# Optimization experiments

Hardware: AMD Instinct MI355X
Metric: run time of the kernel (lower is better)

Reference implementation:

```python
import jax, jax.numpy as jnp
import numpy as np

H = 768       # hidden_dim
NH = 12       # num_heads
HD = H // NH  # head_dim = 64


def setup_inputs() -> dict:
    key = jax.random.key(0)
    ks = jax.random.split(key, 5)
    scale = 1.0 / np.sqrt(H)
    x = jax.random.normal(ks[0], (16, 1024, H), dtype=jnp.float32)
    W_qkv = jax.random.normal(ks[1], (H, 3 * H), dtype=jnp.float32) * scale
    b_qkv = jnp.zeros((3 * H,), dtype=jnp.float32)
    W_proj = jax.random.normal(ks[2], (H, H), dtype=jnp.float32) * scale
    b_proj = jnp.zeros((H,), dtype=jnp.float32)
    return {"x": x, "W_qkv": W_qkv, "b_qkv": b_qkv, "W_proj": W_proj, "b_proj": b_proj}


def reference(x, W_qkv, b_qkv, W_proj, b_proj):
    bsz, seq_len, hidden = x.shape
    qkv = x @ W_qkv + b_qkv                              # [B,S,3H]
    q, k, v = jnp.split(qkv, 3, axis=-1)
    def heads(t):
        return t.reshape(bsz, seq_len, NH, HD).transpose(0, 2, 1, 3)  # [B,NH,S,HD]
    q, k, v = heads(q), heads(k), heads(v)
    scores = jnp.einsum('bhqd,bhkd->bhqk', q, k) / jnp.sqrt(jnp.float32(HD))
    causal = jnp.tril(jnp.ones((seq_len, seq_len), dtype=bool))
    scores = jnp.where(causal, scores, jnp.finfo(scores.dtype).min)
    attn = jax.nn.softmax(scores, axis=-1)
    out = jnp.einsum('bhqk,bhkd->bhqd', attn, v)         # [B,NH,S,HD]
    out = out.transpose(0, 2, 1, 3).reshape(bsz, seq_len, hidden)
    return out @ W_proj + b_proj
```

## Files before the change

### kernel.cpp

```cpp
#include <hip/hip_runtime.h>

#define H 768
#define NH 12
#define HD 64
#define BSZ 16
#define SEQ 1024
#define MTOK (BSZ * SEQ)
#define N3H (3 * H)

typedef __attribute__((ext_vector_type(8))) short bf16x8;
typedef __attribute__((ext_vector_type(4))) float f32x4;
typedef __attribute__((ext_vector_type(16))) float f32x16;
typedef __attribute__((ext_vector_type(8))) unsigned short us8;
typedef __attribute__((ext_vector_type(4))) unsigned short us4;

__device__ __forceinline__ unsigned short f2bf(float f) {
    union { float f; unsigned u; } v; v.f = f;
    unsigned r = v.u + 0x7fffu + ((v.u >> 16) & 1u);
    return (unsigned short)(r >> 16);
}

typedef __attribute__((address_space(1))) const unsigned int gu32_t;
typedef __attribute__((address_space(3))) unsigned int lu32_t;
__device__ __forceinline__ void glds16(const void* g, void* l) {
    __builtin_amdgcn_global_load_lds((gu32_t*)g, (lu32_t*)l, 16, 0, 0);
}

__global__ __launch_bounds__(256) void cvt_bf16(
    const float* __restrict__ in, unsigned short* __restrict__ out, int n)
{
    int i = (blockIdx.x * 256 + threadIdx.x) * 8;
    if (i >= n) return;
    float4 a = *(const float4*)(in + i);
    float4 b = *(const float4*)(in + i + 4);
    us8 o;
    o[0]=f2bf(a.x); o[1]=f2bf(a.y); o[2]=f2bf(a.z); o[3]=f2bf(a.w);
    o[4]=f2bf(b.x); o[5]=f2bf(b.y); o[6]=f2bf(b.z); o[7]=f2bf(b.w);
    *(us8*)(out + i) = o;
}

__global__ __launch_bounds__(256) void tconv_bf16(
    const float* __restrict__ in, unsigned short* __restrict__ out, int Kd, int Nd)
{
    __shared__ float tile[64][65];
    int t = threadIdx.x;
    int n0 = blockIdx.x * 64, k0 = blockIdx.y * 64;
    #pragma unroll
    for (int r = 0; r < 4; ++r) {
        int kl = r * 16 + (t >> 4);
        float4 v = *(const float4*)(&in[(size_t)(k0 + kl) * Nd + n0 + (t & 15) * 4]);
        tile[kl][(t & 15) * 4 + 0] = v.x; tile[kl][(t & 15) * 4 + 1] = v.y;
        tile[kl][(t & 15) * 4 + 2] = v.z; tile[kl][(t & 15) * 4 + 3] = v.w;
    }
    __syncthreads();
    int nl = t >> 2, kc = (t & 3) * 16;
    us8 o0, o1;
    #pragma unroll
    for (int kk = 0; kk < 8; ++kk) o0[kk] = f2bf(tile[kc + kk][nl]);
    #pragma unroll
    for (int kk = 0; kk < 8; ++kk) o1[kk] = f2bf(tile[kc + 8 + kk][nl]);
    size_t ob = (size_t)(n0 + nl) * Kd + k0 + kc;
    *(us8*)(&out[ob]) = o0;
    *(us8*)(&out[ob + 8]) = o1;
}

__global__ __launch_bounds__(256) void gemm_bf16(
    const unsigned short* __restrict__ A, const unsigned short* __restrict__ BT,
    const float* __restrict__ bias, void* __restrict__ Cout,
    int M, int N, int K, int write_f32)
{
    __shared__ char lds[32768];
    char* As = lds;
    char* Bs = lds + 16384;
    const char* Ac = (const char*)A;
    const char* Bc = (const char*)BT;
    int t = threadIdx.x;
    int l = t & 63, w = t >> 6;
    int l16 = l & 15, l4 = l >> 4;
    int wm = w >> 1, wn = w & 1;

    int chunk = (int)gridDim.x >> 3;
    int lin = (blockIdx.x & 7) * chunk + (blockIdx.x >> 3);
    int nbx = N >> 7;
    int bx = lin % nbx, by = lin / nbx;
    int rowBase = by * 128, colBase = bx * 128;

    f32x4 acc[4][4];
    #pragma unroll
    for (int i = 0; i < 4; ++i)
        #pragma unroll
        for (int j = 0; j < 4; ++j) acc[i][j] = (f32x4){0, 0, 0, 0};

    for (int k0 = 0; k0 < K; k0 += 64) {
        #pragma unroll
        for (int i = 0; i < 4; ++i) {
            int c = t + i * 256;
            int row = c >> 3;
            int src = ((c & 7) * 16) ^ ((row & 7) << 4);
            glds16(Ac + ((size_t)(rowBase + row) * K + k0) * 2 + src, As + c * 16);
            glds16(Bc + ((size_t)(colBase + row) * K + k0) * 2 + src, Bs + c * 16);
        }
        asm volatile("s_waitcnt vmcnt(0)" ::: "memory");
        __builtin_amdgcn_s_barrier();

        #pragma unroll
        for (int kh = 0; kh < 2; ++kh) {
            bf16x8 af[4], bfr[4];
            #pragma unroll
            for (int mi = 0; mi < 4; ++mi) {
                int row = wm * 64 + mi * 16 + l16;
                af[mi] = *(const bf16x8*)(As + row * 128 + ((l4 * 16 + kh * 64) ^ ((row & 7) << 4)));
            }
            #pragma unroll
            for (int ni = 0; ni < 4; ++ni) {
                int row = wn * 64 + ni * 16 + l16;
                bfr[ni] = *(const bf16x8*)(Bs + row * 128 + ((l4 * 16 + kh * 64) ^ ((row & 7) << 4)));
            }
            #pragma unroll
            for (int mi = 0; mi < 4; ++mi)
                #pragma unroll
                for (int ni = 0; ni < 4; ++ni)
                    acc[mi][ni] = __builtin_amdgcn_mfma_f32_16x16x32_bf16(
                        af[mi], bfr[ni], acc[mi][ni], 0, 0, 0);
        }
        __builtin_amdgcn_s_barrier();
    }

    #pragma unroll
    for (int ni = 0; ni < 4; ++ni) {
        int col = colBase + wn * 64 + ni * 16 + l16;
        float bb = bias ? bias[col] : 0.f;
        #pragma unroll
        for (int mi = 0; mi < 4; ++mi) {
            #pragma unroll
            for (int j = 0; j < 4; ++j) {
                int row = rowBase + wm * 64 + mi * 16 + l4 * 4 + j;
                float v = acc[mi][ni][j] + bb;
                if (write_f32) ((float*)Cout)[(size_t)row * N + col] = v;
                else ((unsigned short*)Cout)[(size_t)row * N + col] = f2bf(v);
            }
        }
    }
}

__global__ __launch_bounds__(256) void vtrans(
    const unsigned short* __restrict__ qkvb, unsigned short* __restrict__ vt)
{
    __shared__ char tile[64 * 128];
    int t = threadIdx.x;
    int st = blockIdx.x, h = blockIdx.y, b = blockIdx.z;
    int s0 = st * 64;
    {
        int s = t >> 2, dc = (t & 3) * 16;
        size_t g = (size_t)(b * SEQ + s0 + s) * N3H + 2 * H + h * HD + dc;
        us8 v0 = *(const us8*)(&qkvb[g]);
        us8 v1 = *(const us8*)(&qkvb[g + 8]);
        *(us8*)(tile + s * 128 + ((dc * 2) ^ ((s & 7) << 4))) = v0;
        *(us8*)(tile + s * 128 + ((dc * 2 + 16) ^ ((s & 7) << 4))) = v1;
    }
    __syncthreads();
    int d = t >> 2, sc = (t & 3) * 16;
    us8 o0, o1;
    #pragma unroll
    for (int kk = 0; kk < 8; ++kk) {
        int s = sc + kk;
        o0[kk] = *(const unsigned short*)(tile + s * 128 + ((d * 2) ^ ((s & 7) << 4)));
    }
    #pragma unroll
    for (int kk = 0; kk < 8; ++kk) {
        int s = sc + 8 + kk;
        o1[kk] = *(const unsigned short*)(tile + s * 128 + ((d * 2) ^ ((s & 7) << 4)));
    }
    size_t ob = ((size_t)((b * NH + h) * 64 + d)) * SEQ + s0 + sc;
    *(us8*)(&vt[ob]) = o0;
    *(us8*)(&vt[ob + 8]) = o1;
}

__global__ __launch_bounds__(256, 4) void attn_mfma(
    const unsigned short* __restrict__ qkvb,
    const unsigned short* __restrict__ vt,
    unsigned short* __restrict__ aout)
{
    __shared__ char lds[32768];
    char* Kbuf = lds;
    char* Vbuf = lds + 16384;
    int t = threadIdx.x;
    int l = t & 63, w = t >> 6;
    int l31 = l & 31, b5 = l >> 5;

    int lin = ((blockIdx.x & 7) * 192) + (blockIdx.x >> 3);
    int qb = 7 - (lin & 7);
    int bh = lin >> 3;
    int h = bh % NH, b = bh / NH;

    int wq = qb * 128 + w * 32;
    int sw31 = (l31 & 7) << 4;
    int nt = 2 * qb + 2;
    int bhh = b * NH + h;
    const char* qkvc = (const char*)qkvb;
    const char* vtc  = (const char*)vt;

    bf16x8 qB[4];
    {
        const unsigned short* qrow =
            qkvb + (size_t)(b * SEQ + wq + l31) * N3H + h * HD + b5 * 8;
        #pragma unroll
        for (int m = 0; m < 4; ++m) qB[m] = *(const bf16x8*)(qrow + m * 16);
    }

    auto STAGE = [&](int kt, int bi) {
        #pragma unroll
        for (int i = 0; i < 2; ++i) {
            int c = t + i * 256;
            int row = c >> 3;
            int src = ((c & 7) * 16) ^ ((row & 7) << 4);
            glds16(qkvc + ((size_t)(b * SEQ + kt * 64 + row) * N3H + H + h * HD) * 2 + src,
                   Kbuf + bi * 8192 + c * 16);
        }
        #pragma unroll
        for (int i = 0; i < 2; ++i) {
            int c = t + i * 256;
            int row = c >> 3;
            int src = ((c & 7) * 16) ^ ((row & 7) << 4);
            glds16(vtc + (((size_t)(bhh * 64 + row)) * SEQ + kt * 64) * 2 + src,
                   Vbuf + bi * 8192 + c * 16);
        }
    };

    STAGE(0, 0);
    __syncthreads();

    f32x16 o0, o1;
    #pragma unroll
    for (int r = 0; r < 16; ++r) { o0[r] = 0.f; o1[r] = 0.f; }
    float mrun = -1e30f, lrun = 0.f;

    for (int kt = 0; kt < nt; ++kt) {
        int bi = kt & 1;
        if (kt + 1 < nt) {
            STAGE(kt + 1, bi ^ 1);
            asm volatile("s_waitcnt vmcnt(4)" ::: "memory");
        } else {
            asm volatile("s_waitcnt vmcnt(0)" ::: "memory");
        }
        __builtin_amdgcn_s_barrier();

        int ktbase = kt * 64;
        if (ktbase <= wq + 31) {
            const char* Kb = Kbuf + bi * 8192;
            const char* Vb = Vbuf + bi * 8192;

            f32x16 s[2];
            __builtin_amdgcn_s_setprio(1);
            #pragma unroll
            for (int st2 = 0; st2 < 2; ++st2) {
                f32x16 acc;
                #pragma unroll
                for (int r = 0; r < 16; ++r) acc[r] = 0.f;
                #pragma unroll
                for (int m = 0; m < 4; ++m) {
                    int row = st2 * 32 + l31;
                    bf16x8 kf = *(const bf16x8*)(Kb + row * 128 + ((m * 32 + b5 * 16) ^ sw31));
                    acc = __builtin_amdgcn_mfma_f32_32x32x16_bf16(kf, qB[m], acc, 0, 0, 0);
                }
                s[st2] = acc;
            }
            __builtin_amdgcn_s_setprio(0);

            if (ktbase + 63 > wq) {
                int q = wq + l31;
                #pragma unroll
                for (int st2 = 0; st2 < 2; ++st2)
                    #pragma unroll
                    for (int r = 0; r < 16; ++r) {
                        int key = ktbase + st2 * 32 + (r & 3) + 8 * (r >> 2) + 4 * b5;
                        if (key > q) s[st2][r] = -3e38f;
                    }
            }

            float mx = s[0][0];
            #pragma unroll
            for (int r = 1; r < 16; ++r) mx = fmaxf(mx, s[0][r]);
            #pragma unroll
            for (int r = 0; r < 16; ++r) mx = fmaxf(mx, s[1][r]);
            mx = fmaxf(mx, __shfl_xor(mx, 32, 64));
            float mnew = fmaxf(mrun, mx * 0.125f);
            float sc = __expf(mrun - mnew);
            mrun = mnew;
            float rs = 0.f;
            #pragma unroll
            for (int st2 = 0; st2 < 2; ++st2)
                #pragma unroll
                for (int r = 0; r < 16; ++r) {
                    float p = __expf(fmaf(s[st2][r], 0.125f, -mnew));
                    s[st2][r] = p;
                    rs += p;
                }
            rs += __shfl_xor(rs, 32, 64);
            lrun = lrun * sc + rs;
            #pragma unroll
            for (int r = 0; r < 16; ++r) { o0[r] *= sc; o1[r] *= sc; }

            bf16x8 pB[4];
            #pragma unroll
            for (int wd = 0; wd < 4; ++wd) {
                int st2 = wd >> 1, hf = (wd & 1) * 8;
                unsigned pk0 = (unsigned)f2bf(s[st2][hf + 0]) | ((unsigned)f2bf(s[st2][hf + 1]) << 16);
                unsigned pk1 = (unsigned)f2bf(s[st2][hf + 2]) | ((unsigned)f2bf(s[st2][hf + 3]) << 16);
                unsigned pk2 = (unsigned)f2bf(s[st2][hf + 4]) | ((unsigned)f2bf(s[st2][hf + 5]) << 16);
                unsigned pk3 = (unsigned)f2bf(s[st2][hf + 6]) | ((unsigned)f2bf(s[st2][hf + 7]) << 16);
                unsigned snd0 = b5 ? pk0 : pk2;
                unsigned snd1 = b5 ? pk1 : pk3;
                unsigned r0 = (unsigned)__shfl_xor((int)snd0, 32, 64);
                unsigned r1 = (unsigned)__shfl_xor((int)snd1, 32, 64);
                union { unsigned u[4]; bf16x8 v; } cvt;
                cvt.u[0] = b5 ? r0 : pk0;
                cvt.u[1] = b5 ? r1 : pk1;
                cvt.u[2] = b5 ? pk2 : r0;
                cvt.u[3] = b5 ? pk3 : r1;
                pB[wd] = cvt.v;
            }

            __builtin_amdgcn_s_setprio(1);
            #pragma unroll
            for (int wd = 0; wd < 4; ++wd) {
                bf16x8 v0 = *(const bf16x8*)(Vb + l31 * 128 + ((wd * 32 + b5 * 16) ^ sw31));
                o0 = __builtin_amdgcn_mfma_f32_32x32x16_bf16(v0, pB[wd], o0, 0, 0, 0);
                bf16x8 v1 = *(const bf16x8*)(Vb + (32 + l31) * 128 + ((wd * 32 + b5 * 16) ^ sw31));
                o1 = __builtin_amdgcn_mfma_f32_32x32x16_bf16(v1, pB[wd], o1, 0, 0, 0);
            }
            __builtin_amdgcn_s_setprio(0);
        }
        __builtin_amdgcn_s_barrier();
    }

    float inv = 1.f / lrun;
    size_t tok = (size_t)(b * SEQ + wq + l31);
    #pragma unroll
    for (int g = 0; g < 4; ++g) {
        us4 w0, w1;
        #pragma unroll
        for (int j = 0; j < 4; ++j) {
            w0[j] = f2bf(o0[g * 4 + j] * inv);
            w1[j] = f2bf(o1[g * 4 + j] * inv);
        }
        int d0 = g * 8 + b5 * 4;
        *(us4*)(&aout[tok * H + h * HD + d0]) = w0;
        *(us4*)(&aout[tok * H + h * HD + 32 + d0]) = w1;
    }
}

extern "C" void kernel_launch(void* const* d_in, const int* in_sizes, int n_in,
                              void* d_out, int out_size, void* d_ws, size_t ws_size,
                              hipStream_t stream) {
    const float* x      = (const float*)d_in[0];
    const float* W_qkv  = (const float*)d_in[1];
    const float* b_qkv  = (const float*)d_in[2];
    const float* W_proj = (const float*)d_in[3];
    const float* b_proj = (const float*)d_in[4];
    float* outp = (float*)d_out;

    char* ws = (char*)d_ws;
    unsigned short* xbf    = (unsigned short*)ws;  ws += (size_t)MTOK * H * 2;
    unsigned short* wqkvT  = (unsigned short*)ws;  ws += (size_t)N3H * H * 2;
    unsigned short* wprojT = (unsigned short*)ws;  ws += (size_t)H * H * 2;
    unsigned short* qkvb   = (unsigned short*)ws;  ws += (size_t)MTOK * N3H * 2;
    unsigned short* vtb    = (unsigned short*)ws;  ws += (size_t)BSZ * NH * 64 * SEQ * 2;
    unsigned short* aob    = (unsigned short*)ws;

    cvt_bf16<<<(MTOK * H) / (256 * 8), 256, 0, stream>>>(x, xbf, MTOK * H);
    tconv_bf16<<<dim3(N3H / 64, H / 64), 256, 0, stream>>>(W_qkv, wqkvT, H, N3H);
    tconv_bf16<<<dim3(H / 64, H / 64), 256, 0, stream>>>(W_proj, wprojT, H, H);

    gemm_bf16<<<(N3H / 128) * (MTOK / 128), 256, 0, stream>>>(
        xbf, wqkvT, b_qkv, qkvb, MTOK, N3H, H, 0);

    vtrans<<<dim3(SEQ / 64, NH, BSZ), 256, 0, stream>>>(qkvb, vtb);

    attn_mfma<<<(SEQ / 128) * NH * BSZ, 256, 0, stream>>>(qkvb, vtb, aob);

    gemm_bf16<<<(H / 128) * (MTOK / 128), 256, 0, stream>>>(
        aob, wprojT, b_proj, (void*)outp, MTOK, H, H, 1);
}
```

Measured before the change: 317.8 us.

## Double-buffer GEMM LDS loads, fold Q scaling into GEMM, lazy softmax rescale

The GEMM now double-buffers its LDS tiles, so the next K-tile's global-to-LDS loads are issued before the MFMAs on the current tile, and it waits only on the older loads. The QKV GEMM epilogue multiplies Q columns by 1/sqrt(HD), which removes the per-score scaling in attention. The attention softmax skips the running-max rescale of the output and row sum unless some lane's max grew by more than a threshold, trading bounded exp growth for fewer multiplies. LDS per GEMM block doubles to 64KB, which may reduce occupancy.

```diff
diff --git a/kernel.cpp b/kernel.cpp
--- a/kernel.cpp
+++ b/kernel.cpp
@@ -67,11 +67,9 @@
 __global__ __launch_bounds__(256) void gemm_bf16(
     const unsigned short* __restrict__ A, const unsigned short* __restrict__ BT,
     const float* __restrict__ bias, void* __restrict__ Cout,
-    int M, int N, int K, int write_f32)
+    int M, int N, int K, int write_f32, int qscale_end)
 {
-    __shared__ char lds[32768];
-    char* As = lds;
-    char* Bs = lds + 16384;
+    __shared__ char lds[65536];
     const char* Ac = (const char*)A;
     const char* Bc = (const char*)BT;
     int t = threadIdx.x;
@@ -91,7 +89,9 @@
         #pragma unroll
         for (int j = 0; j < 4; ++j) acc[i][j] = (f32x4){0, 0, 0, 0};
 
-    for (int k0 = 0; k0 < K; k0 += 64) {
+    auto STAGE = [&](int k0, int bi) {
+        char* As = lds + bi * 32768;
+        char* Bs = As + 16384;
         #pragma unroll
         for (int i = 0; i < 4; ++i) {
             int c = t + i * 256;
@@ -100,9 +100,22 @@
             glds16(Ac + ((size_t)(rowBase + row) * K + k0) * 2 + src, As + c * 16);
             glds16(Bc + ((size_t)(colBase + row) * K + k0) * 2 + src, Bs + c * 16);
         }
-        asm volatile("s_waitcnt vmcnt(0)" ::: "memory");
+    };
+
+    STAGE(0, 0);
+    int nk = K >> 6;
+    for (int kt = 0; kt < nk; ++kt) {
+        int bi = kt & 1;
+        if (kt + 1 < nk) {
+            STAGE((kt + 1) << 6, bi ^ 1);
+            asm volatile("s_waitcnt vmcnt(8)" ::: "memory");
+        } else {
+            asm volatile("s_waitcnt vmcnt(0)" ::: "memory");
+        }
         __builtin_amdgcn_s_barrier();
 
+        const char* As = lds + bi * 32768;
+        const char* Bs = As + 16384;
         #pragma unroll
         for (int kh = 0; kh < 2; ++kh) {
             bf16x8 af[4], bfr[4];
@@ -130,12 +143,13 @@
     for (int ni = 0; ni < 4; ++ni) {
         int col = colBase + wn * 64 + ni * 16 + l16;
         float bb = bias ? bias[col] : 0.f;
+        float mul = (col < qscale_end) ? 0.125f : 1.0f;
         #pragma unroll
         for (int mi = 0; mi < 4; ++mi) {
             #pragma unroll
             for (int j = 0; j < 4; ++j) {
                 int row = rowBase + wm * 64 + mi * 16 + l4 * 4 + j;
-                float v = acc[mi][ni][j] + bb;
+                float v = (acc[mi][ni][j] + bb) * mul;
                 if (write_f32) ((float*)Cout)[(size_t)row * N + col] = v;
                 else ((unsigned short*)Cout)[(size_t)row * N + col] = f2bf(v);
             }
@@ -284,22 +298,25 @@
             #pragma unroll
             for (int r = 0; r < 16; ++r) mx = fmaxf(mx, s[1][r]);
             mx = fmaxf(mx, __shfl_xor(mx, 32, 64));
-            float mnew = fmaxf(mrun, mx * 0.125f);
-            float sc = __expf(mrun - mnew);
-            mrun = mnew;
+            if (!__all(mx - mrun <= 8.f)) {
+                float mnew = fmaxf(mrun, mx);
+                float sc = __expf(mrun - mnew);
+                mrun = mnew;
+                lrun *= sc;
+                #pragma unroll
+                for (int r = 0; r < 16; ++r) { o0[r] *= sc; o1[r] *= sc; }
+            }
             float rs = 0.f;
             #pragma unroll
             for (int st2 = 0; st2 < 2; ++st2)
                 #pragma unroll
                 for (int r = 0; r < 16; ++r) {
-                    float p = __expf(fmaf(s[st2][r], 0.125f, -mnew));
+                    float p = __expf(s[st2][r] - mrun);
                     s[st2][r] = p;
                     rs += p;
                 }
             rs += __shfl_xor(rs, 32, 64);
-            lrun = lrun * sc + rs;
-            #pragma unroll
-            for (int r = 0; r < 16; ++r) { o0[r] *= sc; o1[r] *= sc; }
+            lrun += rs;
 
             bf16x8 pB[4];
             #pragma unroll
@@ -373,12 +390,12 @@
     tconv_bf16<<<dim3(H / 64, H / 64), 256, 0, stream>>>(W_proj, wprojT, H, H);
 
     gemm_bf16<<<(N3H / 128) * (MTOK / 128), 256, 0, stream>>>(
-        xbf, wqkvT, b_qkv, qkvb, MTOK, N3H, H, 0);
+        xbf, wqkvT, b_qkv, qkvb, MTOK, N3H, H, 0, H);
 
     vtrans<<<dim3(SEQ / 64, NH, BSZ), 256, 0, stream>>>(qkvb, vtb);
 
     attn_mfma<<<(SEQ / 128) * NH * BSZ, 256, 0, stream>>>(qkvb, vtb, aob);
 
     gemm_bf16<<<(H / 128) * (MTOK / 128), 256, 0, stream>>>(
-        aob, wprojT, b_proj, (void*)outp, MTOK, H, H, 1);
-}
+        aob, wprojT, b_proj, (void*)outp, MTOK, H, H, 1, 0);
+}
```

Result: faster. 311.1 us (-2.1%).
